# Kernel optimization log

Measured on AMD Instinct MI355X. Metric: run time of the kernel, lower is better.

## Reference

```python
import jax, jax.numpy as jnp
import numpy as np

OUT_H, OUT_W, GRID_SIZE = 256, 192, 5
N = GRID_SIZE * GRID_SIZE
BATCH = 64


def _make_constants():
    ax = np.linspace(-1.0, 1.0, GRID_SIZE)
    P_Y, P_X = np.meshgrid(ax, ax)
    P_X = P_X.reshape(-1).astype(np.float64)  # (N,)
    P_Y = P_Y.reshape(-1).astype(np.float64)
    d2 = (P_X[:, None] - P_X[None, :]) ** 2 + (P_Y[:, None] - P_Y[None, :]) ** 2
    d2[d2 == 0] = 1.0
    K = d2 * np.log(d2)
    P = np.stack([np.ones(N), P_X, P_Y], axis=1)  # (N,3)
    L = np.block([[K, P], [P.T, np.zeros((3, 3))]])  # (N+3, N+3)
    Li = np.linalg.inv(L).astype(np.float32)
    grid_X, grid_Y = np.meshgrid(np.linspace(-1, 1, OUT_W), np.linspace(-1, 1, OUT_H))
    return (P_X.astype(np.float32), P_Y.astype(np.float32), Li,
            grid_X.astype(np.float32), grid_Y.astype(np.float32))


_PX, _PY, _LI, _GX, _GY = _make_constants()


def setup_inputs() -> dict:
    key = jax.random.key(0)
    theta = jax.random.normal(key, (BATCH, 2 * N), dtype=jnp.float32) * 0.1
    return {"theta": theta}


def reference(theta) -> jnp.ndarray:
    P_X = jnp.asarray(_PX)          # (N,)
    P_Y = jnp.asarray(_PY)
    Li = jnp.asarray(_LI)           # (N+3, N+3)
    grid_X = jnp.asarray(_GX)       # (H, W)
    grid_Y = jnp.asarray(_GY)

    # Absolute control-point targets
    Q_X = theta[:, :N] + P_X        # (B, N)
    Q_Y = theta[:, N:] + P_Y

    # TPS coefficients: non-affine W (B,N) and affine A (B,3)
    W_X = jnp.einsum('nm,bm->bn', Li[:N, :N], Q_X)
    W_Y = jnp.einsum('nm,bm->bn', Li[:N, :N], Q_Y)
    A_X = jnp.einsum('km,bm->bk', Li[N:, :N], Q_X)  # (B,3): [c, cx, cy]
    A_Y = jnp.einsum('km,bm->bk', Li[N:, :N], Q_Y)

    # RBF kernel U(r^2) = r^2 log(r^2), evaluated per pixel per control point
    d2 = (grid_X[:, :, None] - P_X) ** 2 + (grid_Y[:, :, None] - P_Y) ** 2  # (H,W,N)
    d2 = jnp.where(d2 == 0, jnp.float32(1.0), d2)
    U = d2 * jnp.log(d2)            # (H,W,N)

    rbf_X = jnp.einsum('hwn,bn->bhw', U, W_X)
    rbf_Y = jnp.einsum('hwn,bn->bhw', U, W_Y)

    px = (A_X[:, 0, None, None] + A_X[:, 1, None, None] * grid_X
          + A_X[:, 2, None, None] * grid_Y + rbf_X)  # (B,H,W)
    py = (A_Y[:, 0, None, None] + A_Y[:, 1, None, None] * grid_X
          + A_Y[:, 2, None, None] * grid_Y + rbf_Y)

    return jnp.stack([px, py], axis=3)  # (B,H,W,2)
```

## Files before the change

kernel.cpp:

```cpp
#include <hip/hip_runtime.h>

#define OUT_H 256
#define OUT_W 192
#define HWPIX (OUT_H * OUT_W)
#define BATCH 64

typedef float v2f __attribute__((ext_vector_type(2)));
typedef float v4f __attribute__((ext_vector_type(4)));


constexpr double cx_ln(double x) {
  int e = 0;
  while (x >= 1.5) { x *= 0.5; ++e; }
  while (x < 0.75) { x *= 2.0; --e; }
  double t = (x - 1.0) / (x + 1.0);
  double t2 = t * t, s = 0.0, term = t;
  for (int k = 0; k < 20; ++k) { s += term / (double)(2 * k + 1); term *= t2; }
  return 2.0 * s + (double)e * 0.6931471805599453094172321214581766;
}

struct Consts {
  float li[28][25];
  float cp[2][28];
};

constexpr Consts make_consts() {
  Consts out{};
  double PX[25] = {}, PY[25] = {};
  for (int n = 0; n < 25; ++n) {
    PX[n] = -1.0 + 0.5 * (double)(n / 5);
    PY[n] = -1.0 + 0.5 * (double)(n % 5);
  }
  double M[28][56] = {};
  for (int i = 0; i < 28; ++i)
    for (int j = 0; j < 56; ++j) M[i][j] = 0.0;
  for (int i = 0; i < 25; ++i) {
    for (int j = 0; j < 25; ++j) {
      double dx = PX[i] - PX[j], dy = PY[i] - PY[j];
      double d2 = dx * dx + dy * dy;
      M[i][j] = (d2 == 0.0) ? 0.0 : d2 * cx_ln(d2);
    }
    M[i][25] = 1.0; M[i][26] = PX[i]; M[i][27] = PY[i];
    M[25][i] = 1.0; M[26][i] = PX[i]; M[27][i] = PY[i];
  }
  for (int i = 0; i < 28; ++i) M[i][28 + i] = 1.0;
  for (int k = 0; k < 28; ++k) {
    int piv = k;
    double mx = M[k][k] < 0.0 ? -M[k][k] : M[k][k];
    for (int r = k + 1; r < 28; ++r) {
      double a = M[r][k] < 0.0 ? -M[r][k] : M[r][k];
      if (a > mx) { mx = a; piv = r; }
    }
    if (piv != k)
      for (int j = 0; j < 56; ++j) { double t = M[k][j]; M[k][j] = M[piv][j]; M[piv][j] = t; }
    double inv = 1.0 / M[k][k];
    for (int j = 0; j < 56; ++j) M[k][j] *= inv;
    for (int r = 0; r < 28; ++r) {
      if (r == k) continue;
      double f = M[r][k];
      if (f != 0.0)
        for (int j = 0; j < 56; ++j) M[r][j] -= f * M[k][j];
    }
  }
  for (int k = 0; k < 28; ++k)
    for (int m = 0; m < 25; ++m) out.li[k][m] = (float)M[k][28 + m];
  for (int axis = 0; axis < 2; ++axis)
    for (int k = 0; k < 28; ++k) {
      double s = 0.0;
      for (int m = 0; m < 25; ++m)
        s += (double)out.li[k][m] * (axis ? PY[m] : PX[m]);
      out.cp[axis][k] = (float)s;
    }
  return out;
}

constexpr Consts CC = make_consts();

__device__ constexpr float PXf[25] = {
  -1.f,-1.f,-1.f,-1.f,-1.f, -0.5f,-0.5f,-0.5f,-0.5f,-0.5f,
   0.f, 0.f, 0.f, 0.f, 0.f,  0.5f, 0.5f, 0.5f, 0.5f, 0.5f,
   1.f, 1.f, 1.f, 1.f, 1.f };
__device__ constexpr float PYf[25] = {
  -1.f,-0.5f,0.f,0.5f,1.f, -1.f,-0.5f,0.f,0.5f,1.f,
  -1.f,-0.5f,0.f,0.5f,1.f, -1.f,-0.5f,0.f,0.5f,1.f,
  -1.f,-0.5f,0.f,0.5f,1.f };


__global__ __launch_bounds__(256) void tps_fused(const float* __restrict__ theta,
                                                 v4f* __restrict__ out4) {
  __shared__ float sth[32 * 50];
  __shared__ float sC[32 * 56];
  const int t = threadIdx.x;
  const int pg = blockIdx.x >> 1;
  const int bg = blockIdx.x & 1;

  {
    const float4* g4 = (const float4*)theta + bg * 400;
    float4* s4 = (float4*)sth;
#pragma unroll
    for (int i = 0; i < 2; ++i) {
      int idx = t + i * 256;
      if (idx < 400) s4[idx] = g4[idx];
    }
  }
  __syncthreads();

  {
    const int pair = t & 63;
    const int b = pair >> 1, axis = pair & 1;
    const int kg = t >> 6;
    float th[25];
    const float* src = sth + b * 50 + axis * 25;
#pragma unroll
    for (int m = 0; m < 25; ++m) th[m] = src[m];
#pragma unroll
    for (int j = 0; j < 7; ++j) {
      const int k = kg * 7 + j;
      float acc = CC.cp[axis][k];
#pragma unroll
      for (int m = 0; m < 25; ++m) acc += CC.li[k][m] * th[m];
      sC[b * 56 + k * 2 + axis] = acc;
    }
  }
  __syncthreads();

  const int lane = t & 63;
  const int wv = t >> 6;
  const int p0 = pg * 128 + lane * 2;
  const int w0 = p0 % OUT_W;
  const int h = p0 / OUT_W;
  float gx0 = (float)(-1.0 + (double)w0 * (2.0 / 191.0));
  float gx1 = (float)(-1.0 + (double)(w0 + 1) * (2.0 / 191.0));
  float gy  = (float)(-1.0 + (double)h * (2.0 / 255.0));
  if (w0 + 1 == OUT_W - 1) gx1 = 1.0f;
  if (h == OUT_H - 1) gy = 1.0f;

  float U0[28], U1[28];
#pragma unroll
  for (int n = 0; n < 25; ++n) {
    float dyv = gy - PYf[n];
    float dy2 = dyv * dyv;
    float dx0 = gx0 - PXf[n];
    float dx1 = gx1 - PXf[n];
    float d20 = dx0 * dx0 + dy2;
    float d21 = dx1 * dx1 + dy2;
    float u0 = d20 * __logf(d20);
    float u1 = d21 * __logf(d21);
    U0[n] = (d20 == 0.0f) ? 0.0f : u0;
    U1[n] = (d21 == 0.0f) ? 0.0f : u1;
  }
  U0[25] = 1.0f; U0[26] = gx0; U0[27] = gy;
  U1[25] = 1.0f; U1[26] = gx1; U1[27] = gy;

  const float4* cb = (const float4*)sC + wv * 8 * 14;
  v4f* op = out4 + (size_t)(bg * 32 + wv * 8) * (HWPIX / 2) + (pg * 64 + lane);
#pragma unroll 2
  for (int i = 0; i < 8; ++i) {
    const float4* c4 = cb + i * 14;
    v2f a0 = {0.f, 0.f}, a1 = {0.f, 0.f};
#pragma unroll
    for (int j = 0; j < 14; ++j) {
      float4 c = c4[j];
      v2f c01 = {c.x, c.y};
      v2f c23 = {c.z, c.w};
      v2f u00 = {U0[2 * j], U0[2 * j]};
      v2f u01 = {U0[2 * j + 1], U0[2 * j + 1]};
      v2f u10 = {U1[2 * j], U1[2 * j]};
      v2f u11 = {U1[2 * j + 1], U1[2 * j + 1]};
      a0 = __builtin_elementwise_fma(u00, c01, a0);
      a0 = __builtin_elementwise_fma(u01, c23, a0);
      a1 = __builtin_elementwise_fma(u10, c01, a1);
      a1 = __builtin_elementwise_fma(u11, c23, a1);
    }
    v4f res = {a0.x, a0.y, a1.x, a1.y};
    __builtin_nontemporal_store(res, op + (size_t)i * (HWPIX / 2));
  }
}


extern "C" void kernel_launch(void* const* d_in, const int* in_sizes, int n_in,
                              void* d_out, int out_size, void* d_ws, size_t ws_size,
                              hipStream_t stream) {
  const float* theta = (const float*)d_in[0];
  v4f* out4 = (v4f*)d_out;
  hipLaunchKernelGGL(tps_fused, dim3(768), dim3(256), 0, stream, theta, out4);
}
```

Before: 72.80 us.

## Retile TPS kernel to four pixels by four batches per thread with streamed RBF

Each block now covers 256 pixels and 16 batch entries instead of 128 pixels and 32 batches, so each thread holds four pixels and four batches. RBF values are computed on the fly inside the control-point loop instead of being stored in arrays. This raises the ratio of FMAs to logs and shared-memory loads and removes the need to keep large U arrays in registers. In exchange, each block recomputes more RBF values per batch across the grid, and the 16 accumulators per thread may raise register pressure.

New measurement: 74.27 us. 1.02x slower.

```diff
diff --git a/kernel.cpp b/kernel.cpp
--- a/kernel.cpp
+++ b/kernel.cpp
@@ -85,95 +85,122 @@
   -1.f,-0.5f,0.f,0.5f,1.f, -1.f,-0.5f,0.f,0.5f,1.f,
   -1.f,-0.5f,0.f,0.5f,1.f };
 
+__device__ __forceinline__ float rbf_u(float gx, float gy, int n) {
+  float dx = gx - PXf[n];
+  float dy = gy - PYf[n];
+  float d2 = dx * dx + dy * dy;
+  float u = d2 * __logf(d2);
+  return (d2 == 0.0f) ? 0.0f : u;
+}
+
 
 __global__ __launch_bounds__(256) void tps_fused(const float* __restrict__ theta,
                                                  v4f* __restrict__ out4) {
-  __shared__ float sth[32 * 50];
-  __shared__ float sC[32 * 56];
+  __shared__ float sth[16 * 50];
+  __shared__ float sC[16 * 56];
   const int t = threadIdx.x;
-  const int pg = blockIdx.x >> 1;
-  const int bg = blockIdx.x & 1;
+  const int pg = blockIdx.x >> 2;
+  const int bg = blockIdx.x & 3;
 
   {
-    const float4* g4 = (const float4*)theta + bg * 400;
+    const float4* g4 = (const float4*)theta + bg * 200;
     float4* s4 = (float4*)sth;
-#pragma unroll
-    for (int i = 0; i < 2; ++i) {
-      int idx = t + i * 256;
-      if (idx < 400) s4[idx] = g4[idx];
-    }
+    if (t < 200) s4[t] = g4[t];
   }
   __syncthreads();
 
   {
     const int pair = t & 63;
-    const int b = pair >> 1, axis = pair & 1;
     const int kg = t >> 6;
-    float th[25];
-    const float* src = sth + b * 50 + axis * 25;
-#pragma unroll
-    for (int m = 0; m < 25; ++m) th[m] = src[m];
-#pragma unroll
-    for (int j = 0; j < 7; ++j) {
-      const int k = kg * 7 + j;
-      float acc = CC.cp[axis][k];
-#pragma unroll
-      for (int m = 0; m < 25; ++m) acc += CC.li[k][m] * th[m];
-      sC[b * 56 + k * 2 + axis] = acc;
+    if (pair < 32) {
+      const int b = pair >> 1, axis = pair & 1;
+      float th[25];
+      const float* src = sth + b * 50 + axis * 25;
+#pragma unroll
+      for (int m = 0; m < 25; ++m) th[m] = src[m];
+#pragma unroll
+      for (int j = 0; j < 7; ++j) {
+        const int k = kg * 7 + j;
+        float acc = CC.cp[axis][k];
+#pragma unroll
+        for (int m = 0; m < 25; ++m) acc += CC.li[k][m] * th[m];
+        sC[b * 56 + k * 2 + axis] = acc;
+      }
     }
   }
   __syncthreads();
 
   const int lane = t & 63;
   const int wv = t >> 6;
-  const int p0 = pg * 128 + lane * 2;
-  const int w0 = p0 % OUT_W;
-  const int h = p0 / OUT_W;
-  float gx0 = (float)(-1.0 + (double)w0 * (2.0 / 191.0));
-  float gx1 = (float)(-1.0 + (double)(w0 + 1) * (2.0 / 191.0));
-  float gy  = (float)(-1.0 + (double)h * (2.0 / 255.0));
-  if (w0 + 1 == OUT_W - 1) gx1 = 1.0f;
-  if (h == OUT_H - 1) gy = 1.0f;
-
-  float U0[28], U1[28];
-#pragma unroll
-  for (int n = 0; n < 25; ++n) {
-    float dyv = gy - PYf[n];
-    float dy2 = dyv * dyv;
-    float dx0 = gx0 - PXf[n];
-    float dx1 = gx1 - PXf[n];
-    float d20 = dx0 * dx0 + dy2;
-    float d21 = dx1 * dx1 + dy2;
-    float u0 = d20 * __logf(d20);
-    float u1 = d21 * __logf(d21);
-    U0[n] = (d20 == 0.0f) ? 0.0f : u0;
-    U1[n] = (d21 == 0.0f) ? 0.0f : u1;
-  }
-  U0[25] = 1.0f; U0[26] = gx0; U0[27] = gy;
-  U1[25] = 1.0f; U1[26] = gx1; U1[27] = gy;
-
-  const float4* cb = (const float4*)sC + wv * 8 * 14;
-  v4f* op = out4 + (size_t)(bg * 32 + wv * 8) * (HWPIX / 2) + (pg * 64 + lane);
-#pragma unroll 2
-  for (int i = 0; i < 8; ++i) {
-    const float4* c4 = cb + i * 14;
-    v2f a0 = {0.f, 0.f}, a1 = {0.f, 0.f};
-#pragma unroll
-    for (int j = 0; j < 14; ++j) {
-      float4 c = c4[j];
+  const int pA = pg * 256 + 2 * lane;
+  const int pB = pA + 128;
+  const int wA = pA % OUT_W, hA = pA / OUT_W;
+  const int wB = pB % OUT_W, hB = pB / OUT_W;
+
+  float gxA0 = (float)(-1.0 + (double)wA * (2.0 / 191.0));
+  float gxA1 = (wA + 1 == OUT_W - 1) ? 1.0f
+             : (float)(-1.0 + (double)(wA + 1) * (2.0 / 191.0));
+  float gyA  = (hA == OUT_H - 1) ? 1.0f
+             : (float)(-1.0 + (double)hA * (2.0 / 255.0));
+  float gxB0 = (float)(-1.0 + (double)wB * (2.0 / 191.0));
+  float gxB1 = (wB + 1 == OUT_W - 1) ? 1.0f
+             : (float)(-1.0 + (double)(wB + 1) * (2.0 / 191.0));
+  float gyB  = (hB == OUT_H - 1) ? 1.0f
+             : (float)(-1.0 + (double)hB * (2.0 / 255.0));
+
+  const float4* cb = (const float4*)sC + (wv * 4) * 14;
+  v4f* opA = out4 + (size_t)(bg * 16 + wv * 4) * (HWPIX / 2) + (pg * 128 + lane);
+
+  v2f aA0[4], aA1[4], aB0[4], aB1[4];
+#pragma unroll
+  for (int b = 0; b < 4; ++b) {
+    aA0[b] = (v2f){0.f, 0.f}; aA1[b] = (v2f){0.f, 0.f};
+    aB0[b] = (v2f){0.f, 0.f}; aB1[b] = (v2f){0.f, 0.f};
+  }
+
+#pragma unroll
+  for (int j = 0; j < 14; ++j) {
+    float uA00, uA01, uA10, uA11, uB00, uB01, uB10, uB11;
+    if (j < 12) {
+      uA00 = rbf_u(gxA0, gyA, 2 * j); uA01 = rbf_u(gxA0, gyA, 2 * j + 1);
+      uA10 = rbf_u(gxA1, gyA, 2 * j); uA11 = rbf_u(gxA1, gyA, 2 * j + 1);
+      uB00 = rbf_u(gxB0, gyB, 2 * j); uB01 = rbf_u(gxB0, gyB, 2 * j + 1);
+      uB10 = rbf_u(gxB1, gyB, 2 * j); uB11 = rbf_u(gxB1, gyB, 2 * j + 1);
+    } else if (j == 12) {
+      uA00 = rbf_u(gxA0, gyA, 24); uA01 = 1.0f;
+      uA10 = rbf_u(gxA1, gyA, 24); uA11 = 1.0f;
+      uB00 = rbf_u(gxB0, gyB, 24); uB01 = 1.0f;
+      uB10 = rbf_u(gxB1, gyB, 24); uB11 = 1.0f;
+    } else {
+      uA00 = gxA0; uA01 = gyA;  uA10 = gxA1; uA11 = gyA;
+      uB00 = gxB0; uB01 = gyB;  uB10 = gxB1; uB11 = gyB;
+    }
+#pragma unroll
+    for (int b = 0; b < 4; ++b) {
+      float4 c = cb[b * 14 + j];
       v2f c01 = {c.x, c.y};
       v2f c23 = {c.z, c.w};
-      v2f u00 = {U0[2 * j], U0[2 * j]};
-      v2f u01 = {U0[2 * j + 1], U0[2 * j + 1]};
-      v2f u10 = {U1[2 * j], U1[2 * j]};
-      v2f u11 = {U1[2 * j + 1], U1[2 * j + 1]};
-      a0 = __builtin_elementwise_fma(u00, c01, a0);
-      a0 = __builtin_elementwise_fma(u01, c23, a0);
-      a1 = __builtin_elementwise_fma(u10, c01, a1);
-      a1 = __builtin_elementwise_fma(u11, c23, a1);
-    }
-    v4f res = {a0.x, a0.y, a1.x, a1.y};
-    __builtin_nontemporal_store(res, op + (size_t)i * (HWPIX / 2));
+      v2f vA00 = {uA00, uA00}, vA01 = {uA01, uA01};
+      v2f vA10 = {uA10, uA10}, vA11 = {uA11, uA11};
+      v2f vB00 = {uB00, uB00}, vB01 = {uB01, uB01};
+      v2f vB10 = {uB10, uB10}, vB11 = {uB11, uB11};
+      aA0[b] = __builtin_elementwise_fma(vA00, c01, aA0[b]);
+      aA0[b] = __builtin_elementwise_fma(vA01, c23, aA0[b]);
+      aA1[b] = __builtin_elementwise_fma(vA10, c01, aA1[b]);
+      aA1[b] = __builtin_elementwise_fma(vA11, c23, aA1[b]);
+      aB0[b] = __builtin_elementwise_fma(vB00, c01, aB0[b]);
+      aB0[b] = __builtin_elementwise_fma(vB01, c23, aB0[b]);
+      aB1[b] = __builtin_elementwise_fma(vB10, c01, aB1[b]);
+      aB1[b] = __builtin_elementwise_fma(vB11, c23, aB1[b]);
+    }
+  }
+
+#pragma unroll
+  for (int b = 0; b < 4; ++b) {
+    v4f rA = {aA0[b].x, aA0[b].y, aA1[b].x, aA1[b].y};
+    __builtin_nontemporal_store(rA, opA + (size_t)b * (HWPIX / 2));
+    v4f rB = {aB0[b].x, aB0[b].y, aB1[b].x, aB1[b].y};
+    __builtin_nontemporal_store(rB, opA + 64 + (size_t)b * (HWPIX / 2));
   }
 }
 
```
